# Performance work log

Measured on AMD Instinct MI355X. Metric: run time of the kernel, lower is better.

Reference implementation:

```python
import jax, jax.numpy as jnp
import numpy as np

NUM_PROJS = 7
BLOCK_SIZE = 256   # key block size
SAMPLE_SIZE = 256  # residual sampled keys


def _gray_perm(n):
    # AngularLSH._unit_hamming_distance_array: Gray-code bucket permutation
    a = np.array([0, 1], dtype=np.int32)
    for i in range(1, n):
        a = np.concatenate([a, a[::-1] + 2 ** i])
    return a

PERM = jnp.asarray(_gray_perm(NUM_PROJS))
ENC = jnp.asarray(2 ** np.arange(NUM_PROJS), dtype=jnp.int32)


def lsh_hash(x, proj_dir):
    # sign-bit angular LSH -> Gray-code bucket id, [B,H,N]
    bits = (jnp.einsum('bhnd,dr->bhnr', x, proj_dir) > 0).astype(jnp.int32)
    return PERM[(bits * ENC).sum(-1)]


def exact_attention(q, k, v, scale, bias=None):
    s = jnp.einsum('...qd,...kd->...qk', q, k) * scale
    if bias is not None:
        s = s + bias
    lse = jax.nn.logsumexp(s, axis=-1, keepdims=True)
    attn = jnp.einsum('...qk,...kd->...qd', jnp.exp(s - lse), v)
    return attn, lse


def add_self_attentions(a1, l1, a2, l2):
    # stable online-softmax combination of two attention partials
    c = jax.nn.sigmoid(l1 - l2)  # = exp(l1)/(exp(l1)+exp(l2))
    return c * a1 + (1.0 - c) * a2, jnp.logaddexp(l1, l2)


def gather_seq(x, idx):
    # x: [B,H,N,D], idx: [B,H,S] -> [B,H,S,D]
    return jnp.take_along_axis(x, idx[..., None], axis=2)


def hyper_attention(query, key, value, proj_dir, sampled_set):
    B, H, Nq, D = query.shape
    Nk = key.shape[2]
    scale = D ** -0.5
    # --- LSH bucket sort of queries and keys (stable, matches torch.sort stable=True) ---
    q_idx = jnp.argsort(lsh_hash(query, proj_dir), axis=2, stable=True)
    k_idx = jnp.argsort(lsh_hash(key, proj_dir), axis=2, stable=True)
    q_idx_inv = jnp.argsort(q_idx, axis=2, stable=True)
    q_s = gather_seq(query, q_idx)
    k_s = gather_seq(key, k_idx)
    v_s = gather_seq(value, k_idx)
    # --- block-diagonal attention over LSH-sorted blocks ---
    nb = Nk // BLOCK_SIZE          # 32 blocks
    qbs = Nq // nb                 # query block size (== 256 here)
    attn_b, lse_b = exact_attention(
        q_s.reshape(B, H, nb, qbs, D),
        k_s.reshape(B, H, nb, BLOCK_SIZE, D),
        v_s.reshape(B, H, nb, BLOCK_SIZE, D),
        scale)
    attn_b = attn_b.reshape(B, H, Nq, D)
    lse_b = lse_b.reshape(B, H, Nq, 1)
    # --- residual: uniformly sampled keys, importance weight Nk/SAMPLE_SIZE ---
    k_sub = gather_seq(k_s, sampled_set)
    v_sub = gather_seq(v_s, sampled_set)
    q_pos = jnp.arange(Nq) // qbs                    # [Nq] query block ids
    s_blk = sampled_set // BLOCK_SIZE                # [B,H,S] sampled key block ids
    overlap = q_pos[None, None, :, None] == s_blk[:, :, None, :]  # [B,H,Nq,S]
    bias = jnp.where(overlap, jnp.finfo(query.dtype).min, 0.0).astype(query.dtype)
    attn_r, lse_r = exact_attention(q_s, k_sub, v_sub, scale, bias)
    lse_r = lse_r + jnp.asarray(np.log(Nk / SAMPLE_SIZE), lse_r.dtype)
    # --- combine partials via online LSE, then unsort queries ---
    attn, lse = add_self_attentions(attn_b, lse_b, attn_r, lse_r)
    attn = gather_seq(attn, q_idx_inv)
    return attn


def setup_inputs() -> dict:
    key = jax.random.key(0)
    kq, kk, kv, kp, ks = jax.random.split(key, 5)
    B, H, N, D = 2, 16, 8192, 64
    return {
        'query': jax.random.normal(kq, (B, H, N, D), jnp.float32),
        'key': jax.random.normal(kk, (B, H, N, D), jnp.float32),
        'value': jax.random.normal(kv, (B, H, N, D), jnp.float32),
        'proj_dir': jax.random.normal(kp, (D, NUM_PROJS), jnp.float32),
        'sampled_set': jax.random.randint(ks, (B, H, SAMPLE_SIZE), 0, N),
    }


def reference(query, key, value, proj_dir, sampled_set):
    return hyper_attention(query, key, value, proj_dir, sampled_set)
```

## Files before the change

kernel.cpp:

```cpp
#include <hip/hip_runtime.h>

#define BHX   32
#define NSEQ  8192
#define NMASK 8191
#define DIM   64
#define NPROJ 7
#define NBUCK 128
#define NBLK  32
#define QBS   256
#define SSIZE 256
#define LOG32 3.4657359027997265f
#define KPAD  72

typedef unsigned short u16;
typedef unsigned int   u32;
typedef __attribute__((ext_vector_type(8))) short bf16x8;
typedef __attribute__((ext_vector_type(4))) float f32x4;

union B8U { u32 u[4]; bf16x8 v; };

__device__ __forceinline__ u16 f2bf(float f){
    u32 u = __float_as_uint(f);
    u32 r = u + 0x7fffu + ((u >> 16) & 1u);
    return (u16)(r >> 16);
}
__device__ __forceinline__ u32 pk2(float a, float b){
    return (u32)f2bf(a) | ((u32)f2bf(b) << 16);
}
__device__ __forceinline__ f32x4 mfma16(bf16x8 a, bf16x8 b, f32x4 c){
    return __builtin_amdgcn_mfma_f32_16x16x32_bf16(a, b, c, 0, 0, 0);
}

__global__ __launch_bounds__(256) void hash_sort_kernel(
    const float* __restrict__ qg, const float* __restrict__ kg,
    const float* __restrict__ projg,
    u16* __restrict__ qidx, u16* __restrict__ kidx)
{
    const int bh = blockIdx.y;
    const float* __restrict__ x = blockIdx.x ? kg : qg;
    u16* __restrict__ idx       = blockIdx.x ? kidx : qidx;

    __shared__ float projs[NPROJ][DIM];
    __shared__ unsigned char bkts[NSEQ];
    __shared__ u16 hist[NBUCK][130];
    __shared__ int tot[NBUCK];
    __shared__ int base[NBUCK];

    const int t = threadIdx.x;
    if (t < 112) {
        #pragma unroll
        for (int u = 0; u < 4; u++) {
            int e = t * 4 + u;
            int d = e / NPROJ, r = e % NPROJ;
            projs[r][d] = projg[e];
        }
    }
    u32* hz = (u32*)&hist[0][0];
    for (int z = t; z < (NBUCK * 130) / 2; z += 256) hz[z] = 0u;
    __syncthreads();

    const size_t bhN = (size_t)bh * NSEQ;
    for (int i = 0; i < 32; i++) {
        int n = t * 32 + i;
        const float4* row = (const float4*)(x + (bhN + n) * DIM);
        float dot[NPROJ];
        #pragma unroll
        for (int r = 0; r < NPROJ; r++) dot[r] = 0.0f;
        #pragma unroll
        for (int c = 0; c < 16; c++) {
            float4 w = row[c];
            float f[4] = {w.x, w.y, w.z, w.w};
            #pragma unroll
            for (int u = 0; u < 4; u++) {
                float xv = f[u];
                int d = c * 4 + u;
                #pragma unroll
                for (int r = 0; r < NPROJ; r++) dot[r] += xv * projs[r][d];
            }
        }
        int code = 0;
        #pragma unroll
        for (int r = 0; r < NPROJ; r++) code |= (dot[r] > 0.0f ? 1 : 0) << r;
        bkts[n] = (unsigned char)(code ^ (code >> 1));
    }
    __syncthreads();

    if (t < NBUCK) {
        for (int i = 0; i < 64; i++) hist[bkts[t * 64 + i]][t]++;
    }
    __syncthreads();

    if (t < NBUCK) {
        u32 run = 0;
        for (int c = 0; c < 128; c++) {
            u32 v = hist[t][c];
            hist[t][c] = (u16)run;
            run += v;
        }
        tot[t] = (int)run;
    }
    __syncthreads();
    if (t == 0) {
        int run = 0;
        for (int b = 0; b < NBUCK; b++) { base[b] = run; run += tot[b]; }
    }
    __syncthreads();

    if (t < NBUCK) {
        for (int i = 0; i < 64; i++) {
            int n = t * 64 + i;
            int b = bkts[n];
            int pos = base[b] + hist[b][t];
            hist[b][t]++;
            idx[bhN + pos] = (u16)n;
        }
    }
}

__global__ __launch_bounds__(256, 2) void attn_mfma(
    const float* __restrict__ qg, const float* __restrict__ kg,
    const float* __restrict__ vg,
    const u16* __restrict__ qidx, const u16* __restrict__ kidx,
    const int* __restrict__ samp,
    float* __restrict__ outg)
{
    __shared__ u16  Ks[64 * KPAD];
    __shared__ u16  Vt[64 * KPAD];
    __shared__ u16  Ps[4 * 64 * KPAD];
    __shared__ float addv[64];

    const int qb = blockIdx.x, bh = blockIdx.y, t = threadIdx.x;
    const int w = t >> 6, lane = t & 63, c = lane & 15, g = lane >> 4;
    const size_t bhN = (size_t)bh * NSEQ;

    int qi[4];
    bf16x8 qf[4][2];
    #pragma unroll
    for (int qt = 0; qt < 4; qt++) {
        qi[qt] = ((int)qidx[bhN + qb * QBS + w * 64 + qt * 16 + c]) & NMASK;
        const float* qr = qg + (bhN + (size_t)qi[qt]) * DIM;
        #pragma unroll
        for (int dk = 0; dk < 2; dk++) {
            int d0 = dk * 32 + g * 8;
            float4 x = *(const float4*)(qr + d0);
            float4 y = *(const float4*)(qr + d0 + 4);
            B8U f;
            f.u[0] = pk2(x.x * 0.125f, x.y * 0.125f);
            f.u[1] = pk2(x.z * 0.125f, x.w * 0.125f);
            f.u[2] = pk2(y.x * 0.125f, y.y * 0.125f);
            f.u[3] = pk2(y.z * 0.125f, y.w * 0.125f);
            qf[qt][dk] = f.v;
        }
    }

    f32x4 O[4][4];
    #pragma unroll
    for (int dt = 0; dt < 4; dt++)
        #pragma unroll
        for (int qt = 0; qt < 4; qt++) O[dt][qt] = (f32x4)0.0f;
    float m[4] = {-1e30f, -1e30f, -1e30f, -1e30f};
    float l[4] = {0.0f, 0.0f, 0.0f, 0.0f};

    for (int cc = 0; cc < 8; cc++) {
        __syncthreads();
        {
            int s = t >> 2, seg = (t & 3) * 16;
            int grow; float add;
            if (cc < 4) {
                grow = ((int)kidx[bhN + qb * QBS + cc * 64 + s]) & NMASK;
                add  = 0.0f;
            } else {
                int sidx = samp[bh * SSIZE + (cc - 4) * 64 + s] & NMASK;
                grow = ((int)kidx[bhN + sidx]) & NMASK;
                add  = ((sidx >> 8) == qb) ? -1e30f : LOG32;
            }
            const float4* kr = (const float4*)(kg + (bhN + (size_t)grow) * DIM + seg);
            float4 a = kr[0], b = kr[1], e = kr[2], d = kr[3];
            u32* dst = (u32*)&Ks[s * KPAD + seg];
            dst[0] = pk2(a.x, a.y); dst[1] = pk2(a.z, a.w);
            dst[2] = pk2(b.x, b.y); dst[3] = pk2(b.z, b.w);
            dst[4] = pk2(e.x, e.y); dst[5] = pk2(e.z, e.w);
            dst[6] = pk2(d.x, d.y); dst[7] = pk2(d.z, d.w);
            const float4* vr = (const float4*)(vg + (bhN + (size_t)grow) * DIM + seg);
            float4 va = vr[0], vb = vr[1], vc = vr[2], vd = vr[3];
            float vv[16] = {va.x, va.y, va.z, va.w, vb.x, vb.y, vb.z, vb.w,
                            vc.x, vc.y, vc.z, vc.w, vd.x, vd.y, vd.z, vd.w};
            #pragma unroll
            for (int i = 0; i < 16; i++) Vt[(seg + i) * KPAD + s] = f2bf(vv[i]);
            if ((t & 3) == 0) addv[s] = add;
        }
        __syncthreads();

        f32x4 addn[4];
        #pragma unroll
        for (int kt = 0; kt < 4; kt++)
            addn[kt] = *(const f32x4*)&addv[kt * 16 + g * 4];

        bf16x8 ka[4][2];
        #pragma unroll
        for (int kt = 0; kt < 4; kt++)
            #pragma unroll
            for (int dk = 0; dk < 2; dk++)
                ka[kt][dk] = *(const bf16x8*)&Ks[(kt * 16 + c) * KPAD + dk * 32 + g * 8];

        #pragma unroll
        for (int qt = 0; qt < 4; qt++) {
            f32x4 S[4];
            #pragma unroll
            for (int kt = 0; kt < 4; kt++) {
                S[kt] = (f32x4)0.0f;
                S[kt] = mfma16(ka[kt][0], qf[qt][0], S[kt]);
                S[kt] = mfma16(ka[kt][1], qf[qt][1], S[kt]);
            }
            float cmax = -1e30f;
            #pragma unroll
            for (int kt = 0; kt < 4; kt++)
                #pragma unroll
                for (int r = 0; r < 4; r++)
                    cmax = fmaxf(cmax, S[kt][r] + addn[kt][r]);
            cmax = fmaxf(cmax, __shfl_xor(cmax, 16));
            cmax = fmaxf(cmax, __shfl_xor(cmax, 32));
            float mnew  = fmaxf(m[qt], cmax);
            float alpha = __expf(m[qt] - mnew);
            m[qt] = mnew;
            float lsum = 0.0f;
            u16* prow = &Ps[(size_t)(w * 64 + qt * 16 + c) * KPAD];
            #pragma unroll
            for (int kt = 0; kt < 4; kt++) {
                float p0 = __expf(S[kt][0] + addn[kt][0] - mnew);
                float p1 = __expf(S[kt][1] + addn[kt][1] - mnew);
                float p2 = __expf(S[kt][2] + addn[kt][2] - mnew);
                float p3 = __expf(S[kt][3] + addn[kt][3] - mnew);
                lsum += (p0 + p1) + (p2 + p3);
                u32* pw = (u32*)&prow[kt * 16 + g * 4];
                pw[0] = pk2(p0, p1);
                pw[1] = pk2(p2, p3);
            }
            lsum += __shfl_xor(lsum, 16);
            lsum += __shfl_xor(lsum, 32);
            l[qt] = l[qt] * alpha + lsum;
            #pragma unroll
            for (int dt = 0; dt < 4; dt++) O[dt][qt] *= alpha;
        }

        #pragma unroll
        for (int kk = 0; kk < 2; kk++) {
            bf16x8 vfr[4], pfr[4];
            #pragma unroll
            for (int dt = 0; dt < 4; dt++)
                vfr[dt] = *(const bf16x8*)&Vt[(dt * 16 + c) * KPAD + kk * 32 + g * 8];
            #pragma unroll
            for (int qt = 0; qt < 4; qt++)
                pfr[qt] = *(const bf16x8*)&Ps[(size_t)(w * 64 + qt * 16 + c) * KPAD + kk * 32 + g * 8];
            #pragma unroll
            for (int dt = 0; dt < 4; dt++)
                #pragma unroll
                for (int qt = 0; qt < 4; qt++)
                    O[dt][qt] = mfma16(vfr[dt], pfr[qt], O[dt][qt]);
        }
    }

    #pragma unroll
    for (int qt = 0; qt < 4; qt++) {
        float inv = 1.0f / fmaxf(l[qt], 1e-30f);
        float* orow = outg + (bhN + (size_t)qi[qt]) * DIM;
        #pragma unroll
        for (int dt = 0; dt < 4; dt++) {
            f32x4 o = O[dt][qt] * inv;
            *(f32x4*)(orow + dt * 16 + g * 4) = o;
        }
    }
}

extern "C" void kernel_launch(void* const* d_in, const int* in_sizes, int n_in,
                              void* d_out, int out_size, void* d_ws, size_t ws_size,
                              hipStream_t stream)
{
    const float* qg   = (const float*)d_in[0];
    const float* kg   = (const float*)d_in[1];
    const float* vg   = (const float*)d_in[2];
    const float* pg   = (const float*)d_in[3];
    const int*   samp = (const int*)d_in[4];
    float* outg = (float*)d_out;

    u16* qidx = (u16*)d_ws;
    u16* kidx = qidx + BHX * NSEQ;

    hipLaunchKernelGGL(hash_sort_kernel, dim3(2, BHX), dim3(256), 0, stream,
                       qg, kg, pg, qidx, kidx);
    hipLaunchKernelGGL(attn_mfma, dim3(NBLK, BHX), dim3(256), 0, stream,
                       qg, kg, vg, qidx, kidx, samp, outg);
}
```

Before: 364.0 us.

## Split hashing and sorting into separate kernels to raise hash parallelism

The fused hash+sort kernel, which ran only 64 workgroups, is split in two. A hash kernel runs 512 workgroups, each thread computing one row's bucket with coalesced row assignment, and writes bucket bytes to workspace. A separate counting-sort kernel uses all 256 threads for the histogram and scatter instead of 128. This adds an extra launch and a global round-trip of the bucket bytes, plus a larger workspace requirement.

New measurement: 314.2 us. -13.7%, faster.

```diff
diff --git a/kernel.cpp b/kernel.cpp
--- a/kernel.cpp
+++ b/kernel.cpp
@@ -14,6 +14,7 @@
 
 typedef unsigned short u16;
 typedef unsigned int   u32;
+typedef unsigned char  u8;
 typedef __attribute__((ext_vector_type(8))) short bf16x8;
 typedef __attribute__((ext_vector_type(4))) float f32x4;
 
@@ -31,37 +32,30 @@
     return __builtin_amdgcn_mfma_f32_16x16x32_bf16(a, b, c, 0, 0, 0);
 }
 
-__global__ __launch_bounds__(256) void hash_sort_kernel(
+__global__ __launch_bounds__(256) void hash_kernel(
     const float* __restrict__ qg, const float* __restrict__ kg,
     const float* __restrict__ projg,
-    u16* __restrict__ qidx, u16* __restrict__ kidx)
+    u8* __restrict__ bkt)
 {
-    const int bh = blockIdx.y;
-    const float* __restrict__ x = blockIdx.x ? kg : qg;
-    u16* __restrict__ idx       = blockIdx.x ? kidx : qidx;
+    const int slab = blockIdx.x, bh = blockIdx.y, tz = blockIdx.z;
+    const float* __restrict__ x = tz ? kg : qg;
+    u8* __restrict__ ob = bkt + ((size_t)tz * BHX + bh) * NSEQ;
 
     __shared__ float projs[NPROJ][DIM];
-    __shared__ unsigned char bkts[NSEQ];
-    __shared__ u16 hist[NBUCK][130];
-    __shared__ int tot[NBUCK];
-    __shared__ int base[NBUCK];
-
     const int t = threadIdx.x;
     if (t < 112) {
         #pragma unroll
         for (int u = 0; u < 4; u++) {
             int e = t * 4 + u;
-            int d = e / NPROJ, r = e % NPROJ;
-            projs[r][d] = projg[e];
-        }
-    }
-    u32* hz = (u32*)&hist[0][0];
-    for (int z = t; z < (NBUCK * 130) / 2; z += 256) hz[z] = 0u;
+            projs[e % NPROJ][e / NPROJ] = projg[e];
+        }
+    }
     __syncthreads();
 
     const size_t bhN = (size_t)bh * NSEQ;
-    for (int i = 0; i < 32; i++) {
-        int n = t * 32 + i;
+    #pragma unroll
+    for (int j = 0; j < 4; j++) {
+        int n = slab * 1024 + j * 256 + t;
         const float4* row = (const float4*)(x + (bhN + n) * DIM);
         float dot[NPROJ];
         #pragma unroll
@@ -81,18 +75,41 @@
         int code = 0;
         #pragma unroll
         for (int r = 0; r < NPROJ; r++) code |= (dot[r] > 0.0f ? 1 : 0) << r;
-        bkts[n] = (unsigned char)(code ^ (code >> 1));
-    }
-    __syncthreads();
-
-    if (t < NBUCK) {
-        for (int i = 0; i < 64; i++) hist[bkts[t * 64 + i]][t]++;
-    }
+        ob[n] = (u8)(code ^ (code >> 1));
+    }
+}
+
+__global__ __launch_bounds__(256) void sort_kernel(
+    const u8* __restrict__ bkt,
+    u16* __restrict__ qidx, u16* __restrict__ kidx)
+{
+    const int bh = blockIdx.x, tz = blockIdx.y;
+    const u8* __restrict__ ib = bkt + ((size_t)tz * BHX + bh) * NSEQ;
+    u16* __restrict__ idx = (tz ? kidx : qidx) + (size_t)bh * NSEQ;
+
+    __shared__ u8  lb[NSEQ];
+    __shared__ u16 hist[NBUCK][258];
+    __shared__ int base[NBUCK];
+    __shared__ int tot[NBUCK];
+
+    const int t = threadIdx.x;
+    {
+        const uint4* src = (const uint4*)ib;
+        uint4* dst = (uint4*)lb;
+        dst[t] = src[t];
+        dst[256 + t] = src[256 + t];
+    }
+    u32* hz = (u32*)&hist[0][0];
+    for (int z = t; z < (NBUCK * 258) / 2; z += 256) hz[z] = 0u;
+    __syncthreads();
+
+    #pragma unroll 4
+    for (int i = 0; i < 32; i++) hist[lb[t * 32 + i]][t]++;
     __syncthreads();
 
     if (t < NBUCK) {
         u32 run = 0;
-        for (int c = 0; c < 128; c++) {
+        for (int c = 0; c < 256; c++) {
             u32 v = hist[t][c];
             hist[t][c] = (u16)run;
             run += v;
@@ -106,14 +123,13 @@
     }
     __syncthreads();
 
-    if (t < NBUCK) {
-        for (int i = 0; i < 64; i++) {
-            int n = t * 64 + i;
-            int b = bkts[n];
-            int pos = base[b] + hist[b][t];
-            hist[b][t]++;
-            idx[bhN + pos] = (u16)n;
-        }
+    #pragma unroll 4
+    for (int i = 0; i < 32; i++) {
+        int n = t * 32 + i;
+        int b = lb[n];
+        int pos = base[b] + hist[b][t];
+        hist[b][t]++;
+        idx[pos] = (u16)n;
     }
 }
 
@@ -285,9 +301,12 @@
 
     u16* qidx = (u16*)d_ws;
     u16* kidx = qidx + BHX * NSEQ;
-
-    hipLaunchKernelGGL(hash_sort_kernel, dim3(2, BHX), dim3(256), 0, stream,
-                       qg, kg, pg, qidx, kidx);
+    u8*  bkt  = (u8*)(kidx + BHX * NSEQ);
+
+    hipLaunchKernelGGL(hash_kernel, dim3(8, BHX, 2), dim3(256), 0, stream,
+                       qg, kg, pg, bkt);
+    hipLaunchKernelGGL(sort_kernel, dim3(BHX, 2), dim3(256), 0, stream,
+                       bkt, qidx, kidx);
     hipLaunchKernelGGL(attn_mfma, dim3(NBLK, BHX), dim3(256), 0, stream,
                        qg, kg, vg, qidx, kidx, samp, outg);
 }
```
